# Optimization experiments

Measured on AMD Instinct MI355X. Metric: run time of the kernel, lower is better.

## Reference

```python
import jax, jax.numpy as jnp
import numpy as np

N_NODES = 100000
N_EDGES = 1000000
D_IN = 64
EDGE_DIM = 16
D_OUT = 64


def setup_inputs() -> dict:
    key = jax.random.key(0)
    ks = jax.random.split(key, 8)
    x = jax.random.normal(ks[0], (N_NODES, D_IN), dtype=jnp.float32)
    edge_attr = jax.random.normal(ks[1], (N_EDGES, EDGE_DIM), dtype=jnp.float32)
    W_e = jax.random.normal(ks[2], (EDGE_DIM, D_IN), dtype=jnp.float32) / np.sqrt(EDGE_DIM)
    b_e = jax.random.normal(ks[3], (D_IN,), dtype=jnp.float32) * 0.01
    W_l = jax.random.normal(ks[4], (D_IN, D_OUT), dtype=jnp.float32) / np.sqrt(D_IN)
    b_l = jax.random.normal(ks[5], (D_OUT,), dtype=jnp.float32) * 0.01
    W_r = jax.random.normal(ks[6], (D_IN, D_OUT), dtype=jnp.float32) / np.sqrt(D_IN)
    edge_index = jax.random.randint(ks[7], (2, N_EDGES), 0, N_NODES, dtype=jnp.int64)
    return {"x": x, "edge_attr": edge_attr, "W_e": W_e, "b_e": b_e,
            "W_l": W_l, "b_l": b_l, "W_r": W_r, "edge_index": edge_index}


def reference(x, edge_attr, W_e, b_e, W_l, b_l, W_r, edge_index):
    # EdgeSAGEConv with edge_agg='add', aggr='mean', root_weight=True
    n = x.shape[0]
    src, dst = edge_index[0], edge_index[1]  # PyG: row0 = source j, row1 = target i
    # message: x_j + map_edges(edge_attr)
    msg = x[src] + (edge_attr @ W_e + b_e)            # [E, D_IN]
    # scatter-mean aggregate at target nodes
    agg = jax.ops.segment_sum(msg, dst, num_segments=n)             # [N, D_IN]
    cnt = jax.ops.segment_sum(jnp.ones((msg.shape[0], 1), msg.dtype), dst,
                              num_segments=n)                        # [N, 1]
    agg = agg / jnp.maximum(cnt, 1.0)
    # lin_l(agg) + lin_r(x)
    return agg @ W_l + b_l + x @ W_r
```

## Files before the change

### kernel.cpp

```cpp
#include <hip/hip_runtime.h>

#define D 64
#define ED 16

__global__ void detect_idx64_kernel(const int* __restrict__ idx32, int* __restrict__ flag)
{
    __shared__ int any;
    if (threadIdx.x == 0) any = 0;
    __syncthreads();
    int v = 0;
    for (int i = threadIdx.x; i < 8192; i += blockDim.x)
        v |= idx32[2 * i + 1];
    if (v) atomicOr(&any, 1);
    __syncthreads();
    if (threadIdx.x == 0) flag[0] = (any == 0) ? 1 : 0;
}

__device__ __forceinline__ int load_idx(const void* p, size_t i, int is64)
{
    return is64 ? (int)((const long long*)p)[i] : ((const int*)p)[i];
}

__global__ void __launch_bounds__(256)
count_kernel(const void* __restrict__ edge_index, const int* __restrict__ flag,
             int* __restrict__ cnt, int n_edges)
{
    const int is64 = flag[0];
    const int stride = gridDim.x * blockDim.x;
    for (int e = blockIdx.x * blockDim.x + threadIdx.x; e < n_edges; e += stride) {
        int dst = load_idx(edge_index, (size_t)n_edges + e, is64);
        atomicAdd(&cnt[dst], 1);
    }
}

__global__ void scan1_kernel(const int* __restrict__ cnt, int* __restrict__ offs,
                             int* __restrict__ bsum, int n)
{
    __shared__ int sd[256];
    const int t = threadIdx.x;
    const int i = blockIdx.x * 256 + t;
    int v = (i < n) ? cnt[i] : 0;
    sd[t] = v;
    __syncthreads();
    for (int off = 1; off < 256; off <<= 1) {
        int add = (t >= off) ? sd[t - off] : 0;
        __syncthreads();
        sd[t] += add;
        __syncthreads();
    }
    if (i < n) offs[i] = sd[t] - v;
    if (t == 255) bsum[blockIdx.x] = sd[t];
}

__global__ void scan2_kernel(int* __restrict__ bsum, int nb)
{
    __shared__ int sd[512];
    const int t = threadIdx.x;
    int v = (t < nb) ? bsum[t] : 0;
    sd[t] = v;
    __syncthreads();
    for (int off = 1; off < 512; off <<= 1) {
        int add = (t >= off) ? sd[t - off] : 0;
        __syncthreads();
        sd[t] += add;
        __syncthreads();
    }
    if (t < nb) bsum[t] = sd[t] - v;
}

__global__ void scan3_kernel(int* __restrict__ offs, int* __restrict__ cursor,
                             const int* __restrict__ bsum, int n, int n_edges)
{
    const int i = blockIdx.x * 256 + threadIdx.x;
    if (i < n) {
        int v = offs[i] + bsum[i >> 8];
        offs[i]   = v;
        cursor[i] = v;
    }
    if (i == 0) offs[n] = n_edges;
}

__global__ void __launch_bounds__(256)
scatter_kernel(const void* __restrict__ edge_index, const int* __restrict__ flag,
               int* __restrict__ cursor, int2* __restrict__ pair, int n_edges)
{
    const int is64 = flag[0];
    const int stride = gridDim.x * blockDim.x;
    for (int e = blockIdx.x * blockDim.x + threadIdx.x; e < n_edges; e += stride) {
        int src = load_idx(edge_index, e, is64);
        int dst = load_idx(edge_index, (size_t)n_edges + e, is64);
        int pos = atomicAdd(&cursor[dst], 1);
        pair[pos] = make_int2(src, e);
    }
}

#define GATHER_X(J)                                                         \
    _Pragma("unroll")                                                       \
    for (int m = 0; m < 16; ++m) {                                          \
        int s = __shfl(p##J.x, m);                                          \
        t##J[m] = (m < nb##J) ? x[(size_t)s * D + lane] : 0.0f;             \
    }

#define GATHER_EA(J)                                                        \
    _Pragma("unroll")                                                       \
    for (int mm = 0; mm < 4; ++mm) {                                        \
        int m = sub + 4 * mm;                                               \
        int eid = __shfl(p##J.y, m);                                        \
        if (m < nb##J) eac##J += edge_attr[(size_t)eid * ED + k16];         \
    }

#define FINISH(J) do {                                                      \
    float xs = 0.0f;                                                        \
    _Pragma("unroll")                                                       \
    for (int m = 0; m < 16; ++m) xs += t##J[m];                             \
    for (int j0 = 16; j0 < deg##J; j0 += 16) {               \
        const int nbt = min(16, deg##J - j0);                               \
        int2 pt = make_int2(0, 0);                                          \
        if (lane < nbt) pt = pair[beg##J + j0 + lane];                      \
        float tt[16];                                                       \
        _Pragma("unroll")                                                   \
        for (int m = 0; m < 16; ++m) {                                      \
            int s = __shfl(pt.x, m);                                        \
            tt[m] = (m < nbt) ? x[(size_t)s * D + lane] : 0.0f;             \
        }                                                                   \
        _Pragma("unroll")                                                   \
        for (int mm = 0; mm < 4; ++mm) {                                    \
            int m = sub + 4 * mm;                                           \
            int eid = __shfl(pt.y, m);                                      \
            if (m < nbt) eac##J += edge_attr[(size_t)eid * ED + k16];       \
        }                                                                   \
        _Pragma("unroll")                                                   \
        for (int m = 0; m < 16; ++m) xs += tt[m];                           \
    }                                                                       \
    float eaf = eac##J + __shfl_xor(eac##J, 16);                            \
    eaf += __shfl_xor(eaf, 32);                                             \
    float acc = xs + (float)deg##J * beL;                                   \
    _Pragma("unroll")                                                       \
    for (int k = 0; k < ED; ++k) acc += __shfl(eaf, k) * Wreg[k];           \
    if (v##J)                                                               \
        agg[(size_t)n##J * D + lane] = acc * (1.0f / fmaxf((float)deg##J, 1.0f)); \
} while (0)

__global__ void
reduce_kernel(const float* __restrict__ x,
              const float* __restrict__ edge_attr,
              const float* __restrict__ W_e,
              const float* __restrict__ b_e,
              const int2* __restrict__ pair,
              const int* __restrict__ offs,
              float* __restrict__ agg,
              int n_nodes)
{
    const int lane = threadIdx.x & 63;
    const int wid  = threadIdx.x >> 6;
    const int sub  = lane >> 4;
    const int k16  = lane & 15;

    float Wreg[ED];
    #pragma unroll
    for (int k = 0; k < ED; ++k) Wreg[k] = W_e[k * D + lane];
    const float beL = b_e[lane];

    const int tw = gridDim.x * 4;
    const int wg = blockIdx.x * 4 + wid;

    for (int k0 = 0; wg + k0 * tw < n_nodes; k0 += 4) {
        const int  n0 = wg + (k0 + 0) * tw;
        const int  n1 = wg + (k0 + 1) * tw;
        const int  n2 = wg + (k0 + 2) * tw;
        const int  n3 = wg + (k0 + 3) * tw;
        const bool v0 = true;
        const bool v1 = n1 < n_nodes;
        const bool v2 = n2 < n_nodes;
        const bool v3 = n3 < n_nodes;
        const int  c1 = v1 ? n1 : 0;
        const int  c2 = v2 ? n2 : 0;
        const int  c3 = v3 ? n3 : 0;

        const int beg0 = offs[n0], end0 = offs[n0 + 1];
        const int beg1 = offs[c1], end1 = offs[c1 + 1];
        const int beg2 = offs[c2], end2 = offs[c2 + 1];
        const int beg3 = offs[c3], end3 = offs[c3 + 1];
        const int deg0 = end0 - beg0;
        const int deg1 = v1 ? (end1 - beg1) : 0;
        const int deg2 = v2 ? (end2 - beg2) : 0;
        const int deg3 = v3 ? (end3 - beg3) : 0;
        const int nb0 = min(deg0, 16);
        const int nb1 = min(deg1, 16);
        const int nb2 = min(deg2, 16);
        const int nb3 = min(deg3, 16);

        int2 p0 = make_int2(0, 0); if (lane < nb0) p0 = pair[beg0 + lane];
        int2 p1 = make_int2(0, 0); if (lane < nb1) p1 = pair[beg1 + lane];
        int2 p2 = make_int2(0, 0); if (lane < nb2) p2 = pair[beg2 + lane];
        int2 p3 = make_int2(0, 0); if (lane < nb3) p3 = pair[beg3 + lane];

        float t0[16], t1[16], t2[16], t3[16];
        float eac0 = 0.0f, eac1 = 0.0f, eac2 = 0.0f, eac3 = 0.0f;
        GATHER_X(0); GATHER_X(1); GATHER_X(2); GATHER_X(3);
        GATHER_EA(0); GATHER_EA(1); GATHER_EA(2); GATHER_EA(3);

        FINISH(0); FINISH(1); FINISH(2); FINISH(3);
    }
}

__global__ void __launch_bounds__(256)
edge_scatter_kernel(const float* __restrict__ x,
                    const float* __restrict__ edge_attr,
                    const float* __restrict__ W_e,
                    const float* __restrict__ b_e,
                    const void* __restrict__ edge_index,
                    const int* __restrict__ flag,
                    float* __restrict__ agg,
                    float* __restrict__ cnt,
                    int n_edges)
{
    __shared__ float We[ED * D];
    __shared__ float be[D];
    for (int i = threadIdx.x; i < ED * D; i += blockDim.x) We[i] = W_e[i];
    if (threadIdx.x < D) be[threadIdx.x] = b_e[threadIdx.x];
    __syncthreads();

    const int is64 = flag[0];
    const int lane = threadIdx.x & 63;
    const int wid  = threadIdx.x >> 6;
    const int estr = gridDim.x * 4;

    for (int e = blockIdx.x * 4 + wid; e < n_edges; e += estr) {
        int src = load_idx(edge_index, e, is64);
        int dst = load_idx(edge_index, (size_t)n_edges + e, is64);
        const float4* ea = (const float4*)(edge_attr + (size_t)e * ED);
        float4 e0 = ea[0], e1 = ea[1], e2 = ea[2], e3 = ea[3];

        float m = be[lane] + x[(size_t)src * D + lane];
        m += e0.x * We[ 0*D + lane] + e0.y * We[ 1*D + lane]
           + e0.z * We[ 2*D + lane] + e0.w * We[ 3*D + lane];
        m += e1.x * We[ 4*D + lane] + e1.y * We[ 5*D + lane]
           + e1.z * We[ 6*D + lane] + e1.w * We[ 7*D + lane];
        m += e2.x * We[ 8*D + lane] + e2.y * We[ 9*D + lane]
           + e2.z * We[10*D + lane] + e2.w * We[11*D + lane];
        m += e3.x * We[12*D + lane] + e3.y * We[13*D + lane]
           + e3.z * We[14*D + lane] + e3.w * We[15*D + lane];

        atomicAdd(&agg[(size_t)dst * D + lane], m);
        if (lane == 0) atomicAdd(&cnt[dst], 1.0f);
    }
}

__global__ void divide_kernel(float* __restrict__ agg, const float* __restrict__ cnt, int n_nodes)
{
    const int i = blockIdx.x * 256 + threadIdx.x;
    if (i < n_nodes * D) {
        float c = cnt[i >> 6];
        agg[i] *= 1.0f / fmaxf(c, 1.0f);
    }
}

#define BM 128
#define BK 32
#define ATP 132

__global__ void __launch_bounds__(256, 4)
node_gemm_kernel(const float* x,
                 const float* agg,
                 const float* __restrict__ W_l,
                 const float* __restrict__ b_l,
                 const float* __restrict__ W_r,
                 float* out,
                 int n_nodes)
{
    __shared__ float AT[BK][ATP];
    __shared__ float Wt[BK][D];

    const int t   = threadIdx.x;
    const int to  = t & 15;
    const int tm  = t >> 4;
    const int base = blockIdx.x * BM;

    float acc[8][4];
    #pragma unroll
    for (int n = 0; n < 8; ++n)
        #pragma unroll
        for (int c = 0; c < 4; ++c) acc[n][c] = 0.0f;

    #pragma unroll 1
    for (int s = 0; s < 4; ++s) {
        const float* src  = (s < 2) ? agg : x;
        const float* Wsrc = (s < 2) ? W_l : W_r;
        const int    k0   = (s & 1) * BK;

        __syncthreads();

        #pragma unroll
        for (int q = 0; q < 4; ++q) {
            const int idx  = t + 256 * q;
            const int node = idx >> 3;
            const int kq   = (idx & 7) * 4;
            float4 v = make_float4(0.f, 0.f, 0.f, 0.f);
            if (base + node < n_nodes)
                v = *(const float4*)(src + (size_t)(base + node) * D + k0 + kq);
            AT[kq + 0][node] = v.x;
            AT[kq + 1][node] = v.y;
            AT[kq + 2][node] = v.z;
            AT[kq + 3][node] = v.w;
        }
        #pragma unroll
        for (int q = 0; q < 2; ++q) {
            const int idx = t + 256 * q;
            const int kk  = idx >> 4;
            const int cq  = (idx & 15) * 4;
            *(float4*)&Wt[kk][cq] = *(const float4*)(Wsrc + (size_t)(k0 + kk) * D + cq);
        }
        __syncthreads();

        #pragma unroll 4
        for (int kk = 0; kk < BK; ++kk) {
            float4 a0 = *(const float4*)&AT[kk][tm * 8];
            float4 a1 = *(const float4*)&AT[kk][tm * 8 + 4];
            float4 w  = *(const float4*)&Wt[kk][to * 4];
            acc[0][0] += a0.x * w.x; acc[0][1] += a0.x * w.y; acc[0][2] += a0.x * w.z; acc[0][3] += a0.x * w.w;
            acc[1][0] += a0.y * w.x; acc[1][1] += a0.y * w.y; acc[1][2] += a0.y * w.z; acc[1][3] += a0.y * w.w;
            acc[2][0] += a0.z * w.x; acc[2][1] += a0.z * w.y; acc[2][2] += a0.z * w.z; acc[2][3] += a0.z * w.w;
            acc[3][0] += a0.w * w.x; acc[3][1] += a0.w * w.y; acc[3][2] += a0.w * w.z; acc[3][3] += a0.w * w.w;
            acc[4][0] += a1.x * w.x; acc[4][1] += a1.x * w.y; acc[4][2] += a1.x * w.z; acc[4][3] += a1.x * w.w;
            acc[5][0] += a1.y * w.x; acc[5][1] += a1.y * w.y; acc[5][2] += a1.y * w.z; acc[5][3] += a1.y * w.w;
            acc[6][0] += a1.z * w.x; acc[6][1] += a1.z * w.y; acc[6][2] += a1.z * w.z; acc[6][3] += a1.z * w.w;
            acc[7][0] += a1.w * w.x; acc[7][1] += a1.w * w.y; acc[7][2] += a1.w * w.z; acc[7][3] += a1.w * w.w;
        }
    }

    const float4 bb = *(const float4*)(b_l + to * 4);
    #pragma unroll
    for (int n = 0; n < 8; ++n) {
        const int node = base + tm * 8 + n;
        if (node < n_nodes) {
            float4 r = make_float4(acc[n][0] + bb.x, acc[n][1] + bb.y,
                                   acc[n][2] + bb.z, acc[n][3] + bb.w);
            *(float4*)(out + (size_t)node * D + to * 4) = r;
        }
    }
}

extern "C" void kernel_launch(void* const* d_in, const int* in_sizes, int n_in,
                              void* d_out, int out_size, void* d_ws, size_t ws_size,
                              hipStream_t stream)
{
    const float* x         = (const float*)d_in[0];
    const float* edge_attr = (const float*)d_in[1];
    const float* W_e       = (const float*)d_in[2];
    const float* b_e       = (const float*)d_in[3];
    const float* W_l       = (const float*)d_in[4];
    const float* b_l       = (const float*)d_in[5];
    const float* W_r       = (const float*)d_in[6];
    const void*  edge_index= d_in[7];

    const int n_nodes = in_sizes[0] / D;
    const int n_edges = in_sizes[1] / ED;

    float* out = (float*)d_out;

    const size_t n_align = ((size_t)n_nodes + 255) & ~(size_t)255;
    const int    NB      = (n_nodes + 255) / 256;
    const size_t o_flag  = 0;
    const size_t o_cnt   = 512;
    const size_t o_offs  = o_cnt  + n_align * 4;
    const size_t o_cur   = o_offs + n_align * 4 + 256;
    const size_t o_bsum  = o_cur  + n_align * 4;
    const size_t o_pair  = (o_bsum + (size_t)NB * 4 + 255) & ~(size_t)255;
    const size_t need    = o_pair + (size_t)n_edges * 8;

    int* flag = (int*)((char*)d_ws + o_flag);

    detect_idx64_kernel<<<1, 256, 0, stream>>>((const int*)edge_index, flag);

    if (need <= ws_size && NB <= 512) {
        int*  cnt    = (int*)((char*)d_ws + o_cnt);
        int*  offs   = (int*)((char*)d_ws + o_offs);
        int*  cursor = (int*)((char*)d_ws + o_cur);
        int*  bsum   = (int*)((char*)d_ws + o_bsum);
        int2* pair   = (int2*)((char*)d_ws + o_pair);

        hipMemsetAsync(cnt, 0, n_align * 4, stream);

        count_kernel<<<2048, 256, 0, stream>>>(edge_index, flag, cnt, n_edges);
        scan1_kernel<<<NB, 256, 0, stream>>>(cnt, offs, bsum, n_nodes);
        scan2_kernel<<<1, 512, 0, stream>>>(bsum, NB);
        scan3_kernel<<<NB, 256, 0, stream>>>(offs, cursor, bsum, n_nodes, n_edges);
        scatter_kernel<<<2048, 256, 0, stream>>>(edge_index, flag, cursor, pair, n_edges);
        reduce_kernel<<<2048, 256, 0, stream>>>(
            x, edge_attr, W_e, b_e, pair, offs, out, n_nodes);
    } else {
        float* cntf = (float*)((char*)d_ws + o_cnt);
        hipMemsetAsync(out, 0, (size_t)out_size * sizeof(float), stream);
        hipMemsetAsync(cntf, 0, (size_t)n_nodes * sizeof(float), stream);
        edge_scatter_kernel<<<4096, 256, 0, stream>>>(
            x, edge_attr, W_e, b_e, edge_index, flag, out, cntf, n_edges);
        divide_kernel<<<(n_nodes * D + 255) / 256, 256, 0, stream>>>(out, cntf, n_nodes);
    }

    node_gemm_kernel<<<(n_nodes + BM - 1) / BM, 256, 0, stream>>>(
        x, out, W_l, b_l, W_r, out, n_nodes);
}
```

Baseline: 286.8 us.

## Inline index-width detection, fold block-sum scan into scan3, reshape reduce node batching

Removes the separate detect kernel by having each kernel check the index width with a wave vote over 64 entries, and removes scan2 by having each scan3 block sum the preceding block totals itself. The reduce kernel now handles two adjacent nodes per wave per iteration instead of four strided nodes, with launch bounds set for two blocks per CU. This cuts two kernel launches and may improve occupancy and offs locality. In exchange, scan3 does redundant prefix work per block, the index-width check samples fewer entries, and each wave has less memory-level parallelism in flight.

```diff
diff --git a/kernel.cpp b/kernel.cpp
--- a/kernel.cpp
+++ b/kernel.cpp
@@ -3,17 +3,10 @@
 #define D 64
 #define ED 16
 
-__global__ void detect_idx64_kernel(const int* __restrict__ idx32, int* __restrict__ flag)
-{
-    __shared__ int any;
-    if (threadIdx.x == 0) any = 0;
-    __syncthreads();
-    int v = 0;
-    for (int i = threadIdx.x; i < 8192; i += blockDim.x)
-        v |= idx32[2 * i + 1];
-    if (v) atomicOr(&any, 1);
-    __syncthreads();
-    if (threadIdx.x == 0) flag[0] = (any == 0) ? 1 : 0;
+__device__ __forceinline__ int detect_is64(const int* __restrict__ idx32)
+{
+    int v = idx32[2 * (threadIdx.x & 63) + 1];
+    return __all(v == 0) ? 1 : 0;
 }
 
 __device__ __forceinline__ int load_idx(const void* p, size_t i, int is64)
@@ -22,10 +15,9 @@
 }
 
 __global__ void __launch_bounds__(256)
-count_kernel(const void* __restrict__ edge_index, const int* __restrict__ flag,
-             int* __restrict__ cnt, int n_edges)
-{
-    const int is64 = flag[0];
+count_kernel(const void* __restrict__ edge_index, int* __restrict__ cnt, int n_edges)
+{
+    const int is64 = detect_is64((const int*)edge_index);
     const int stride = gridDim.x * blockDim.x;
     for (int e = blockIdx.x * blockDim.x + threadIdx.x; e < n_edges; e += stride) {
         int dst = load_idx(edge_index, (size_t)n_edges + e, is64);
@@ -52,28 +44,22 @@
     if (t == 255) bsum[blockIdx.x] = sd[t];
 }
 
-__global__ void scan2_kernel(int* __restrict__ bsum, int nb)
-{
-    __shared__ int sd[512];
-    const int t = threadIdx.x;
-    int v = (t < nb) ? bsum[t] : 0;
-    sd[t] = v;
-    __syncthreads();
-    for (int off = 1; off < 512; off <<= 1) {
-        int add = (t >= off) ? sd[t - off] : 0;
-        __syncthreads();
-        sd[t] += add;
-        __syncthreads();
-    }
-    if (t < nb) bsum[t] = sd[t] - v;
-}
-
 __global__ void scan3_kernel(int* __restrict__ offs, int* __restrict__ cursor,
                              const int* __restrict__ bsum, int n, int n_edges)
 {
+    __shared__ int red[256];
+    int part = 0;
+    for (int j = threadIdx.x; j < blockIdx.x; j += 256) part += bsum[j];
+    red[threadIdx.x] = part;
+    __syncthreads();
+    for (int off = 128; off > 0; off >>= 1) {
+        if (threadIdx.x < off) red[threadIdx.x] += red[threadIdx.x + off];
+        __syncthreads();
+    }
+    const int S = red[0];
     const int i = blockIdx.x * 256 + threadIdx.x;
     if (i < n) {
-        int v = offs[i] + bsum[i >> 8];
+        int v = offs[i] + S;
         offs[i]   = v;
         cursor[i] = v;
     }
@@ -81,10 +67,10 @@
 }
 
 __global__ void __launch_bounds__(256)
-scatter_kernel(const void* __restrict__ edge_index, const int* __restrict__ flag,
+scatter_kernel(const void* __restrict__ edge_index,
                int* __restrict__ cursor, int2* __restrict__ pair, int n_edges)
 {
-    const int is64 = flag[0];
+    const int is64 = detect_is64((const int*)edge_index);
     const int stride = gridDim.x * blockDim.x;
     for (int e = blockIdx.x * blockDim.x + threadIdx.x; e < n_edges; e += stride) {
         int src = load_idx(edge_index, e, is64);
@@ -113,7 +99,7 @@
     float xs = 0.0f;                                                        \
     _Pragma("unroll")                                                       \
     for (int m = 0; m < 16; ++m) xs += t##J[m];                             \
-    for (int j0 = 16; j0 < deg##J; j0 += 16) {               \
+    for (int j0 = 16; j0 < deg##J; j0 += 16) {       \
         const int nbt = min(16, deg##J - j0);                               \
         int2 pt = make_int2(0, 0);                                          \
         if (lane < nbt) pt = pair[beg##J + j0 + lane];                      \
@@ -141,7 +127,7 @@
         agg[(size_t)n##J * D + lane] = acc * (1.0f / fmaxf((float)deg##J, 1.0f)); \
 } while (0)
 
-__global__ void
+__global__ void __launch_bounds__(256, 2)
 reduce_kernel(const float* __restrict__ x,
               const float* __restrict__ edge_attr,
               const float* __restrict__ W_e,
@@ -164,43 +150,31 @@
     const int tw = gridDim.x * 4;
     const int wg = blockIdx.x * 4 + wid;
 
-    for (int k0 = 0; wg + k0 * tw < n_nodes; k0 += 4) {
-        const int  n0 = wg + (k0 + 0) * tw;
-        const int  n1 = wg + (k0 + 1) * tw;
-        const int  n2 = wg + (k0 + 2) * tw;
-        const int  n3 = wg + (k0 + 3) * tw;
+    for (int base = wg * 2; base < n_nodes; base += tw * 2) {
+        const int  n0 = base;
+        const int  n1 = base + 1;
         const bool v0 = true;
         const bool v1 = n1 < n_nodes;
-        const bool v2 = n2 < n_nodes;
-        const bool v3 = n3 < n_nodes;
-        const int  c1 = v1 ? n1 : 0;
-        const int  c2 = v2 ? n2 : 0;
-        const int  c3 = v3 ? n3 : 0;
-
-        const int beg0 = offs[n0], end0 = offs[n0 + 1];
-        const int beg1 = offs[c1], end1 = offs[c1 + 1];
-        const int beg2 = offs[c2], end2 = offs[c2 + 1];
-        const int beg3 = offs[c3], end3 = offs[c3 + 1];
-        const int deg0 = end0 - beg0;
+        const int  c1 = v1 ? n1 : n0;
+
+        const int beg0 = offs[n0];
+        const int mid  = offs[n0 + 1];
+        const int beg1 = offs[c1];
+        const int end1 = offs[c1 + 1];
+        const int deg0 = mid - beg0;
         const int deg1 = v1 ? (end1 - beg1) : 0;
-        const int deg2 = v2 ? (end2 - beg2) : 0;
-        const int deg3 = v3 ? (end3 - beg3) : 0;
         const int nb0 = min(deg0, 16);
         const int nb1 = min(deg1, 16);
-        const int nb2 = min(deg2, 16);
-        const int nb3 = min(deg3, 16);
 
         int2 p0 = make_int2(0, 0); if (lane < nb0) p0 = pair[beg0 + lane];
         int2 p1 = make_int2(0, 0); if (lane < nb1) p1 = pair[beg1 + lane];
-        int2 p2 = make_int2(0, 0); if (lane < nb2) p2 = pair[beg2 + lane];
-        int2 p3 = make_int2(0, 0); if (lane < nb3) p3 = pair[beg3 + lane];
-
-        float t0[16], t1[16], t2[16], t3[16];
-        float eac0 = 0.0f, eac1 = 0.0f, eac2 = 0.0f, eac3 = 0.0f;
-        GATHER_X(0); GATHER_X(1); GATHER_X(2); GATHER_X(3);
-        GATHER_EA(0); GATHER_EA(1); GATHER_EA(2); GATHER_EA(3);
-
-        FINISH(0); FINISH(1); FINISH(2); FINISH(3);
+
+        float t0[16], t1[16];
+        float eac0 = 0.0f, eac1 = 0.0f;
+        GATHER_X(0); GATHER_X(1);
+        GATHER_EA(0); GATHER_EA(1);
+
+        FINISH(0); FINISH(1);
     }
 }
 
@@ -210,7 +184,6 @@
                     const float* __restrict__ W_e,
                     const float* __restrict__ b_e,
                     const void* __restrict__ edge_index,
-                    const int* __restrict__ flag,
                     float* __restrict__ agg,
                     float* __restrict__ cnt,
                     int n_edges)
@@ -221,7 +194,7 @@
     if (threadIdx.x < D) be[threadIdx.x] = b_e[threadIdx.x];
     __syncthreads();
 
-    const int is64 = flag[0];
+    const int is64 = detect_is64((const int*)edge_index);
     const int lane = threadIdx.x & 63;
     const int wid  = threadIdx.x >> 6;
     const int estr = gridDim.x * 4;
@@ -361,19 +334,14 @@
 
     const size_t n_align = ((size_t)n_nodes + 255) & ~(size_t)255;
     const int    NB      = (n_nodes + 255) / 256;
-    const size_t o_flag  = 0;
-    const size_t o_cnt   = 512;
+    const size_t o_cnt   = 0;
     const size_t o_offs  = o_cnt  + n_align * 4;
     const size_t o_cur   = o_offs + n_align * 4 + 256;
     const size_t o_bsum  = o_cur  + n_align * 4;
     const size_t o_pair  = (o_bsum + (size_t)NB * 4 + 255) & ~(size_t)255;
     const size_t need    = o_pair + (size_t)n_edges * 8;
 
-    int* flag = (int*)((char*)d_ws + o_flag);
-
-    detect_idx64_kernel<<<1, 256, 0, stream>>>((const int*)edge_index, flag);
-
-    if (need <= ws_size && NB <= 512) {
+    if (need <= ws_size && NB <= 65536) {
         int*  cnt    = (int*)((char*)d_ws + o_cnt);
         int*  offs   = (int*)((char*)d_ws + o_offs);
         int*  cursor = (int*)((char*)d_ws + o_cur);
@@ -382,11 +350,10 @@
 
         hipMemsetAsync(cnt, 0, n_align * 4, stream);
 
-        count_kernel<<<2048, 256, 0, stream>>>(edge_index, flag, cnt, n_edges);
+        count_kernel<<<2048, 256, 0, stream>>>(edge_index, cnt, n_edges);
         scan1_kernel<<<NB, 256, 0, stream>>>(cnt, offs, bsum, n_nodes);
-        scan2_kernel<<<1, 512, 0, stream>>>(bsum, NB);
         scan3_kernel<<<NB, 256, 0, stream>>>(offs, cursor, bsum, n_nodes, n_edges);
-        scatter_kernel<<<2048, 256, 0, stream>>>(edge_index, flag, cursor, pair, n_edges);
+        scatter_kernel<<<2048, 256, 0, stream>>>(edge_index, cursor, pair, n_edges);
         reduce_kernel<<<2048, 256, 0, stream>>>(
             x, edge_attr, W_e, b_e, pair, offs, out, n_nodes);
     } else {
@@ -394,7 +361,7 @@
         hipMemsetAsync(out, 0, (size_t)out_size * sizeof(float), stream);
         hipMemsetAsync(cntf, 0, (size_t)n_nodes * sizeof(float), stream);
         edge_scatter_kernel<<<4096, 256, 0, stream>>>(
-            x, edge_attr, W_e, b_e, edge_index, flag, out, cntf, n_edges);
+            x, edge_attr, W_e, b_e, edge_index, out, cntf, n_edges);
         divide_kernel<<<(n_nodes * D + 255) / 256, 256, 0, stream>>>(out, cntf, n_nodes);
     }
 
```

Measured after the change: 254.3 us. -11.3%, faster.
